# Kernel tuning notes

Hardware: AMD Instinct MI355X
Metric: run time of the kernel (lower is better)

## Reference

```python
import jax, jax.numpy as jnp
import numpy as np

BATCH = 16384
IN_F = 768
OUT_F = 768
GRID_SIZE = 8           # act_fun.get_size()
GRID_LO, GRID_HI = -2.0, 2.0


def rbf_basis(x):
    """Gaussian RBF spline basis: [b, i] -> [b, a, i]."""
    grid = jnp.linspace(GRID_LO, GRID_HI, GRID_SIZE, dtype=x.dtype)  # [a]
    h = (GRID_HI - GRID_LO) / (GRID_SIZE - 1)
    z = (x[:, None, :] - grid[None, :, None]) / h                    # [b, a, i]
    return jnp.exp(-z * z)


def setup_inputs() -> dict:
    key = jax.random.key(0)
    k1, k2, k3 = jax.random.split(key, 3)
    x = jax.random.normal(k1, (BATCH, IN_F), dtype=jnp.float32)
    # xavier_normal_(gain=0.001): std = 0.001 * sqrt(2 / (fan_in + fan_out))
    std_wb = 0.001 * np.sqrt(2.0 / (IN_F + OUT_F))
    w_b = jax.random.normal(k2, (OUT_F, IN_F), dtype=jnp.float32) * std_wb
    w_s = jnp.ones((OUT_F, IN_F), dtype=jnp.float32)
    c = jax.random.normal(k3, (GRID_SIZE, OUT_F, IN_F), dtype=jnp.float32) * 0.001
    return {"x": x, "w_b": w_b, "w_s": w_s, "c": c}


def reference(x, w_b, w_s, c):
    # Original: sum_i[ (sum_a phi(x)_{bai} c_{aoi}) * w_s_{oi} + silu(x)_{bi} * w_b_{oi} ]
    phi = rbf_basis(x)                       # [b, a, i]
    cw = c * w_s[None, :, :]                 # fold scale into coeffs: [a, o, i]
    spline = jnp.einsum('bai,aoi->bo', phi, cw)   # fused contraction over (a, i)
    res = jax.nn.silu(x) @ w_b.T             # [b, o]
    return spline + res
```

## Files before the change

kernel.cpp:

```cpp
#include <hip/hip_runtime.h>
#include <hip/hip_bf16.h>

#define BATCH 16384
#define INF 768
#define OUTF 768
#define NSLAB 9
#define KTOT (NSLAB * INF)
#define BM 128
#define BN 128
#define BK 64
#define KB_TILES 12
#define NTILES (NSLAB * KB_TILES)

#define LOG2E 1.4426950408889634f
#define EXPM2 0.13533528323661270f

#define TILE_SH 8192
#define IB_SH   8192
#define SLAB_SH (KB_TILES * TILE_SH)

typedef __bf16 bf16x8 __attribute__((ext_vector_type(8)));
typedef float f32x4 __attribute__((ext_vector_type(4)));
typedef unsigned short ushort8v __attribute__((ext_vector_type(8)));

__device__ __forceinline__ unsigned short f2bf(float f) {
  unsigned u = __builtin_bit_cast(unsigned, f);
  u += 0x7fffu + ((u >> 16) & 1u);
  return (unsigned short)(u >> 16);
}

__device__ __forceinline__ unsigned cvt2(float a, float b) {
  __hip_bfloat162 h = __float22bfloat162_rn(make_float2(a, b));
  unsigned r;
  __builtin_memcpy(&r, &h, 4);
  return r;
}

__device__ __forceinline__ bf16x8 pack8(const f32x4 a, const f32x4 b) {
  union { uint4 u; bf16x8 v; } r;
  r.u.x = cvt2(a[0], a[1]); r.u.y = cvt2(a[2], a[3]);
  r.u.z = cvt2(b[0], b[1]); r.u.w = cvt2(b[2], b[3]);
  return r.v;
}

__device__ __forceinline__ void gload_lds16(const void* g, void* l) {
  __builtin_amdgcn_global_load_lds(
      (const __attribute__((address_space(1))) unsigned int*)g,
      (__attribute__((address_space(3))) unsigned int*)l, 16, 0, 0);
}

__global__ __launch_bounds__(256) void build_bext2(
    const float* __restrict__ w_b, const float* __restrict__ w_s,
    const float* __restrict__ c, unsigned short* __restrict__ bt) {
  const int gid = blockIdx.x * 256 + threadIdx.x;
  const int lane = gid & 63;
  const int q = (gid >> 6) & 3;
  const int wv = (gid >> 8) & 3;
  const int tile = gid >> 10;
  const int kt = tile % NTILES;
  const int cbq = tile / NTILES;
  const int a = kt / KB_TILES;
  const int ib = kt - a * KB_TILES;
  const int rg = lane >> 3, chh = lane & 7;
  const int o = cbq * 128 + wv * 32 + q * 8 + rg;
  const int i = ib * 64 + (chh ^ rg) * 8;

  float4 v0, v1;
  if (a < 8) {
    const float* cp = c + ((size_t)(a * OUTF + o)) * INF + i;
    const float* wp = w_s + (size_t)o * INF + i;
    const float4 c0 = *(const float4*)cp, c1 = *(const float4*)(cp + 4);
    const float4 s0 = *(const float4*)wp, s1 = *(const float4*)(wp + 4);
    v0 = make_float4(c0.x * s0.x, c0.y * s0.y, c0.z * s0.z, c0.w * s0.w);
    v1 = make_float4(c1.x * s1.x, c1.y * s1.y, c1.z * s1.z, c1.w * s1.w);
  } else {
    const float* bp = w_b + (size_t)o * INF + i;
    v0 = *(const float4*)bp;
    v1 = *(const float4*)(bp + 4);
  }
  ushort8v r;
  r[0] = f2bf(v0.x); r[1] = f2bf(v0.y); r[2] = f2bf(v0.z); r[3] = f2bf(v0.w);
  r[4] = f2bf(v1.x); r[5] = f2bf(v1.y); r[6] = f2bf(v1.z); r[7] = f2bf(v1.w);
  *(ushort8v*)(bt + (size_t)gid * 8) = r;
}

__global__ __launch_bounds__(256, 2) void kan_gemm7(
    const float* __restrict__ x, const unsigned short* __restrict__ bt,
    float* __restrict__ out) {
  __shared__ unsigned short Bs[3][BN * BK];

  const int orig = blockIdx.x;
  const int bid = (orig & 7) * 96 + (orig >> 3);
  const int cb = bid / (BATCH / BM);
  const int rb = bid - cb * (BATCH / BM);
  const int row0 = rb * BM, col0 = cb * BN;

  const int t = threadIdx.x;
  const int lane = t & 63;
  const int w = t >> 6;
  const int lrow = lane & 15, lhi = lane >> 4;

  f32x4 acc[2][8];
#pragma unroll
  for (int mt = 0; mt < 2; ++mt)
#pragma unroll
    for (int n = 0; n < 8; ++n)
      acc[mt][n] = (f32x4){0.f, 0.f, 0.f, 0.f};

  const unsigned short* gt =
      bt + (size_t)cb * NTILES * TILE_SH + w * 2048 + lane * 8;
  const float* xb = x + (size_t)(row0 + w * 32 + lrow) * INF;

  const int c0 = lhi ^ (lrow & 7);
  const int c1 = (4 + lhi) ^ (lrow & 7);
  const unsigned short* pB0 = &Bs[0][lrow * 64 + c0 * 8];
  const unsigned short* pB1 = &Bs[0][lrow * 64 + c1 * 8];

  f32x4 ph[2][2][2], gg[2][2][2];

  auto stage = [&](const unsigned short* src, int slot) {
#pragma unroll
    for (int q = 0; q < 4; ++q)
      gload_lds16(src + q * 512, &Bs[slot][w * 2048 + q * 512]);
  };

  auto mma_kk = [&](int kk, int slot, bf16x8 af0, bf16x8 af1) {
    const unsigned short* pB = kk ? pB1 : pB0;
#pragma unroll
    for (int n = 0; n < 8; ++n) {
      const bf16x8 b = *(const bf16x8*)(pB + slot * TILE_SH + n * 1024);
      acc[0][n] = __builtin_amdgcn_mfma_f32_16x16x32_bf16(af0, b, acc[0][n], 0, 0, 0);
      acc[1][n] = __builtin_amdgcn_mfma_f32_16x16x32_bf16(af1, b, acc[1][n], 0, 0, 0);
    }
  };

  const unsigned short* gib = gt;
  stage(gib + 8 * SLAB_SH, 0);
  stage(gib, 1);
  asm volatile("s_waitcnt vmcnt(4)" ::: "memory");
  __builtin_amdgcn_s_barrier();
  __builtin_amdgcn_sched_barrier(0);

#pragma clang loop unroll(disable)
  for (int ib = 0; ib < KB_TILES; ++ib) {
    const float* xib = xb + ib * BK;
    const bool last = (ib == KB_TILES - 1);
#pragma unroll
    for (int j = 0; j < 9; ++j) {
      const int slot = j % 3;

      if (j == 0) {
        f32x4 xr[4][2];
#pragma unroll
        for (int g = 0; g < 4; ++g) {
          const float* p = xib + (g >> 1) * 16 * INF + (g & 1) * 32 + lhi * 8;
          xr[g][0] = *(const f32x4*)p;
          xr[g][1] = *(const f32x4*)(p + 4);
        }
        stage(gib + 1 * SLAB_SH, 2);
#pragma unroll
        for (int kk = 0; kk < 2; ++kk) {
          bf16x8 af[2];
#pragma unroll
          for (int mt = 0; mt < 2; ++mt) {
            const f32x4 x0 = xr[mt * 2 + kk][0], x1 = xr[mt * 2 + kk][1];
            f32x4 s0, s1;
#pragma unroll
            for (int e = 0; e < 4; ++e) {
              s0[e] = x0[e] * __builtin_amdgcn_rcpf(
                          1.f + __builtin_amdgcn_exp2f(x0[e] * (-LOG2E)));
              s1[e] = x1[e] * __builtin_amdgcn_rcpf(
                          1.f + __builtin_amdgcn_exp2f(x1[e] * (-LOG2E)));
            }
            af[mt] = pack8(s0, s1);
            const f32x4 z0 = x0 * 1.75f + 3.5f;
            const f32x4 z1 = x1 * 1.75f + 3.5f;
#pragma unroll
            for (int e = 0; e < 4; ++e) {
              ph[mt][kk][0][e] = __builtin_amdgcn_exp2f(-(z0[e] * z0[e]) * LOG2E);
              ph[mt][kk][1][e] = __builtin_amdgcn_exp2f(-(z1[e] * z1[e]) * LOG2E);
              gg[mt][kk][0][e] = __builtin_amdgcn_exp2f(z0[e] * (2.f * LOG2E) - LOG2E);
              gg[mt][kk][1][e] = __builtin_amdgcn_exp2f(z1[e] * (2.f * LOG2E) - LOG2E);
            }
          }
          mma_kk(kk, 0, af[0], af[1]);
        }
      } else {
        if (j <= 6) {
          stage(gib + (j + 1) * SLAB_SH, (j + 2) % 3);
        } else if (!last) {
          if (j == 7) stage(gib + 8 * SLAB_SH + IB_SH, 0);
          else        stage(gib + IB_SH, 1);
        }
#pragma unroll
        for (int kk = 0; kk < 2; ++kk) {
          bf16x8 af[2];
#pragma unroll
          for (int mt = 0; mt < 2; ++mt) {
            af[mt] = pack8(ph[mt][kk][0], ph[mt][kk][1]);
            ph[mt][kk][0] *= gg[mt][kk][0];
            ph[mt][kk][1] *= gg[mt][kk][1];
            gg[mt][kk][0] = gg[mt][kk][0] * EXPM2;
            gg[mt][kk][1] = gg[mt][kk][1] * EXPM2;
          }
          mma_kk(kk, slot, af[0], af[1]);
        }
      }

      if (!last || j < 7) {
        asm volatile("s_waitcnt vmcnt(4)" ::: "memory");
      } else if (j == 7) {
        asm volatile("s_waitcnt vmcnt(0)" ::: "memory");
      }
      if (!(last && j == 8)) {
        __builtin_amdgcn_s_barrier();
        __builtin_amdgcn_sched_barrier(0);
      }
    }
    gib += IB_SH;
  }

#pragma unroll
  for (int mt = 0; mt < 2; ++mt) {
#pragma unroll
    for (int n = 0; n < 8; ++n) {
      const int row = row0 + w * 32 + mt * 16 + lhi * 4;
      const int col = col0 + n * 16 + lrow;
#pragma unroll
      for (int r = 0; r < 4; ++r)
        out[(size_t)(row + r) * OUTF + col] = acc[mt][n][r];
    }
  }
}

__device__ __forceinline__ float phi_f(float x, float g) {
  float z = (x - g) * 1.75f;
  return __expf(-z * z);
}
__device__ __forceinline__ float silu_f(float x) {
  return x / (1.f + __expf(-x));
}

__global__ __launch_bounds__(256, 2) void kan_gemm_fb(
    const float* __restrict__ x, const float* __restrict__ w_b,
    const float* __restrict__ w_s, const float* __restrict__ c,
    float* __restrict__ out) {
  __shared__ unsigned short As[128][72];
  __shared__ unsigned short Bs[128][72];

  const int bid = blockIdx.x;
  const int cbf = bid % (OUTF / 128);
  const int rbf = bid / (OUTF / 128);
  const int row0 = rbf * 128, col0 = cbf * 128;

  const int t = threadIdx.x;
  const int lane = t & 63;
  const int w = t >> 6;
  const int wr = w >> 1, wc = w & 1;
  const int lrow = lane & 15, lhi = lane >> 4;

  f32x4 acc[4][4];
#pragma unroll
  for (int m = 0; m < 4; ++m)
#pragma unroll
    for (int n = 0; n < 4; ++n)
      acc[m][n] = (f32x4){0.f, 0.f, 0.f, 0.f};

  const int rsub = t >> 4;
  const int k4 = t & 15;

  for (int kt = 0; kt < KTOT / 64; ++kt) {
    const int a = kt / (INF / 64);
    const int i0 = (kt % (INF / 64)) * 64;
    const float ga = -2.f + (float)a * (4.f / 7.f);

#pragma unroll
    for (int p = 0; p < 8; ++p) {
      const int r = p * 16 + rsub;
      const float4 xv = *(const float4*)(x + (size_t)(row0 + r) * INF + i0 + k4 * 4);
      ushort4 av;
      if (a < 8) {
        av.x = f2bf(phi_f(xv.x, ga)); av.y = f2bf(phi_f(xv.y, ga));
        av.z = f2bf(phi_f(xv.z, ga)); av.w = f2bf(phi_f(xv.w, ga));
      } else {
        av.x = f2bf(silu_f(xv.x)); av.y = f2bf(silu_f(xv.y));
        av.z = f2bf(silu_f(xv.z)); av.w = f2bf(silu_f(xv.w));
      }
      *(ushort4*)&As[r][k4 * 4] = av;

      ushort4 bv;
      if (a < 8) {
        const float4 cv = *(const float4*)(c + ((size_t)a * OUTF + col0 + r) * INF + i0 + k4 * 4);
        const float4 wv = *(const float4*)(w_s + (size_t)(col0 + r) * INF + i0 + k4 * 4);
        bv.x = f2bf(cv.x * wv.x); bv.y = f2bf(cv.y * wv.y);
        bv.z = f2bf(cv.z * wv.z); bv.w = f2bf(cv.w * wv.w);
      } else {
        const float4 bbv = *(const float4*)(w_b + (size_t)(col0 + r) * INF + i0 + k4 * 4);
        bv.x = f2bf(bbv.x); bv.y = f2bf(bbv.y);
        bv.z = f2bf(bbv.z); bv.w = f2bf(bbv.w);
      }
      *(ushort4*)&Bs[r][k4 * 4] = bv;
    }
    __syncthreads();

#pragma unroll
    for (int kk = 0; kk < 2; ++kk) {
      bf16x8 af[4], bfr[4];
#pragma unroll
      for (int m = 0; m < 4; ++m)
        af[m] = *(const bf16x8*)&As[wr * 64 + m * 16 + lrow][kk * 32 + lhi * 8];
#pragma unroll
      for (int n = 0; n < 4; ++n)
        bfr[n] = *(const bf16x8*)&Bs[wc * 64 + n * 16 + lrow][kk * 32 + lhi * 8];
#pragma unroll
      for (int m = 0; m < 4; ++m)
#pragma unroll
        for (int n = 0; n < 4; ++n)
          acc[m][n] = __builtin_amdgcn_mfma_f32_16x16x32_bf16(af[m], bfr[n], acc[m][n], 0, 0, 0);
    }
    __syncthreads();
  }

#pragma unroll
  for (int m = 0; m < 4; ++m) {
#pragma unroll
    for (int n = 0; n < 4; ++n) {
      const int row = row0 + wr * 64 + m * 16 + lhi * 4;
      const int col = col0 + wc * 64 + n * 16 + lrow;
#pragma unroll
      for (int r = 0; r < 4; ++r)
        out[(size_t)(row + r) * OUTF + col] = acc[m][n][r];
    }
  }
}

extern "C" void kernel_launch(void* const* d_in, const int* in_sizes, int n_in,
                              void* d_out, int out_size, void* d_ws, size_t ws_size,
                              hipStream_t stream) {
  const float* x   = (const float*)d_in[0];
  const float* w_b = (const float*)d_in[1];
  const float* w_s = (const float*)d_in[2];
  const float* c   = (const float*)d_in[3];
  float* out = (float*)d_out;

  const size_t need = (size_t)OUTF * KTOT * sizeof(unsigned short);
  if (ws_size >= need) {
    unsigned short* bt = (unsigned short*)d_ws;
    build_bext2<<<(OUTF * KTOT / 8) / 256, 256, 0, stream>>>(w_b, w_s, c, bt);
    kan_gemm7<<<(BATCH / BM) * (OUTF / BN), 256, 0, stream>>>(x, bt, out);
  } else {
    kan_gemm_fb<<<(BATCH / 128) * (OUTF / 128), 256, 0, stream>>>(x, w_b, w_s, c, out);
  }
}
```

Baseline: 226.9 us.

## Switch GEMM warp tiling to 2x2 grid with 64x64 per-warp tiles

Reorganizes the four warps from 32-row by 128-column strips into a 2x2 arrangement of 64x64 tiles. Each warp now reads half as many B fragments from shared memory per k-step. In exchange, every x row's RBF basis and SiLU values are computed by two warps instead of one, doubling that elementwise exp work. It also doubles the per-thread basis recurrence registers, which raises register pressure under the two-blocks-per-CU bound.

```diff
diff --git a/kernel.cpp b/kernel.cpp
--- a/kernel.cpp
+++ b/kernel.cpp
@@ -84,7 +84,7 @@
   *(ushort8v*)(bt + (size_t)gid * 8) = r;
 }
 
-__global__ __launch_bounds__(256, 2) void kan_gemm7(
+__global__ __launch_bounds__(256, 2) void kan_gemm8(
     const float* __restrict__ x, const unsigned short* __restrict__ bt,
     float* __restrict__ out) {
   __shared__ unsigned short Bs[3][BN * BK];
@@ -98,25 +98,26 @@
   const int t = threadIdx.x;
   const int lane = t & 63;
   const int w = t >> 6;
+  const int wr = w >> 1, wc = w & 1;
   const int lrow = lane & 15, lhi = lane >> 4;
 
-  f32x4 acc[2][8];
-#pragma unroll
-  for (int mt = 0; mt < 2; ++mt)
-#pragma unroll
-    for (int n = 0; n < 8; ++n)
+  f32x4 acc[4][4];
+#pragma unroll
+  for (int mt = 0; mt < 4; ++mt)
+#pragma unroll
+    for (int n = 0; n < 4; ++n)
       acc[mt][n] = (f32x4){0.f, 0.f, 0.f, 0.f};
 
   const unsigned short* gt =
       bt + (size_t)cb * NTILES * TILE_SH + w * 2048 + lane * 8;
-  const float* xb = x + (size_t)(row0 + w * 32 + lrow) * INF;
+  const float* xb = x + (size_t)(row0 + wr * 64 + lrow) * INF;
 
   const int c0 = lhi ^ (lrow & 7);
   const int c1 = (4 + lhi) ^ (lrow & 7);
-  const unsigned short* pB0 = &Bs[0][lrow * 64 + c0 * 8];
-  const unsigned short* pB1 = &Bs[0][lrow * 64 + c1 * 8];
-
-  f32x4 ph[2][2][2], gg[2][2][2];
+  const unsigned short* pB0 = &Bs[0][(wc * 64 + lrow) * 64 + c0 * 8];
+  const unsigned short* pB1 = &Bs[0][(wc * 64 + lrow) * 64 + c1 * 8];
+
+  f32x4 ph[4][2][2], gg[4][2][2];
 
   auto stage = [&](const unsigned short* src, int slot) {
 #pragma unroll
@@ -124,13 +125,14 @@
       gload_lds16(src + q * 512, &Bs[slot][w * 2048 + q * 512]);
   };
 
-  auto mma_kk = [&](int kk, int slot, bf16x8 af0, bf16x8 af1) {
+  auto mma_kk = [&](int kk, int slot, const bf16x8* af) {
     const unsigned short* pB = kk ? pB1 : pB0;
 #pragma unroll
-    for (int n = 0; n < 8; ++n) {
+    for (int n = 0; n < 4; ++n) {
       const bf16x8 b = *(const bf16x8*)(pB + slot * TILE_SH + n * 1024);
-      acc[0][n] = __builtin_amdgcn_mfma_f32_16x16x32_bf16(af0, b, acc[0][n], 0, 0, 0);
-      acc[1][n] = __builtin_amdgcn_mfma_f32_16x16x32_bf16(af1, b, acc[1][n], 0, 0, 0);
+#pragma unroll
+      for (int mt = 0; mt < 4; ++mt)
+        acc[mt][n] = __builtin_amdgcn_mfma_f32_16x16x32_bf16(af[mt], b, acc[mt][n], 0, 0, 0);
     }
   };
 
@@ -150,20 +152,22 @@
       const int slot = j % 3;
 
       if (j == 0) {
-        f32x4 xr[4][2];
-#pragma unroll
-        for (int g = 0; g < 4; ++g) {
-          const float* p = xib + (g >> 1) * 16 * INF + (g & 1) * 32 + lhi * 8;
-          xr[g][0] = *(const f32x4*)p;
-          xr[g][1] = *(const f32x4*)(p + 4);
-        }
+        f32x4 xr[4][2][2];
+#pragma unroll
+        for (int mt = 0; mt < 4; ++mt)
+#pragma unroll
+          for (int kk = 0; kk < 2; ++kk) {
+            const float* p = xib + mt * 16 * INF + kk * 32 + lhi * 8;
+            xr[mt][kk][0] = *(const f32x4*)p;
+            xr[mt][kk][1] = *(const f32x4*)(p + 4);
+          }
         stage(gib + 1 * SLAB_SH, 2);
 #pragma unroll
         for (int kk = 0; kk < 2; ++kk) {
-          bf16x8 af[2];
-#pragma unroll
-          for (int mt = 0; mt < 2; ++mt) {
-            const f32x4 x0 = xr[mt * 2 + kk][0], x1 = xr[mt * 2 + kk][1];
+          bf16x8 af[4];
+#pragma unroll
+          for (int mt = 0; mt < 4; ++mt) {
+            const f32x4 x0 = xr[mt][kk][0], x1 = xr[mt][kk][1];
             f32x4 s0, s1;
 #pragma unroll
             for (int e = 0; e < 4; ++e) {
@@ -183,7 +187,7 @@
               gg[mt][kk][1][e] = __builtin_amdgcn_exp2f(z1[e] * (2.f * LOG2E) - LOG2E);
             }
           }
-          mma_kk(kk, 0, af[0], af[1]);
+          mma_kk(kk, 0, af);
         }
       } else {
         if (j <= 6) {
@@ -194,16 +198,16 @@
         }
 #pragma unroll
         for (int kk = 0; kk < 2; ++kk) {
-          bf16x8 af[2];
-#pragma unroll
-          for (int mt = 0; mt < 2; ++mt) {
+          bf16x8 af[4];
+#pragma unroll
+          for (int mt = 0; mt < 4; ++mt) {
             af[mt] = pack8(ph[mt][kk][0], ph[mt][kk][1]);
             ph[mt][kk][0] *= gg[mt][kk][0];
             ph[mt][kk][1] *= gg[mt][kk][1];
             gg[mt][kk][0] = gg[mt][kk][0] * EXPM2;
             gg[mt][kk][1] = gg[mt][kk][1] * EXPM2;
           }
-          mma_kk(kk, slot, af[0], af[1]);
+          mma_kk(kk, slot, af);
         }
       }
 
@@ -221,11 +225,11 @@
   }
 
 #pragma unroll
-  for (int mt = 0; mt < 2; ++mt) {
-#pragma unroll
-    for (int n = 0; n < 8; ++n) {
-      const int row = row0 + w * 32 + mt * 16 + lhi * 4;
-      const int col = col0 + n * 16 + lrow;
+  for (int mt = 0; mt < 4; ++mt) {
+#pragma unroll
+    for (int n = 0; n < 4; ++n) {
+      const int row = row0 + wr * 64 + mt * 16 + lhi * 4;
+      const int col = col0 + wc * 64 + n * 16 + lrow;
 #pragma unroll
       for (int r = 0; r < 4; ++r)
         out[(size_t)(row + r) * OUTF + col] = acc[mt][n][r];
@@ -347,7 +351,7 @@
   if (ws_size >= need) {
     unsigned short* bt = (unsigned short*)d_ws;
     build_bext2<<<(OUTF * KTOT / 8) / 256, 256, 0, stream>>>(w_b, w_s, c, bt);
-    kan_gemm7<<<(BATCH / BM) * (OUTF / BN), 256, 0, stream>>>(x, bt, out);
+    kan_gemm8<<<(BATCH / BM) * (OUTF / BN), 256, 0, stream>>>(x, bt, out);
   } else {
     kan_gemm_fb<<<(BATCH / 128) * (OUTF / 128), 256, 0, stream>>>(x, w_b, w_s, c, out);
   }
```

Result: slower. 459.7 us (+102.6%).

## Software-pipeline A-fragment generation and x loads one step ahead of MFMAs

Applied to the files above, without the earlier changes.

Moves the x loads for the next K-block into the last slab step and computes the SiLU/RBF A-fragments for the next step after the current MFMAs, so the basis math for step j+1 overlaps the matrix ops of step j instead of sitting serially in front of them. The x load latency is also hidden behind the j==8 MFMAs rather than exposed at j==0. It also replaces the bf16 pair conversion with a single v_cvt_pk_bf16_f32 inline asm instruction. The cost is extra live registers for the prefetched x values and the precomputed fragments, which could pressure the 2-waves-per-SIMD occupancy target.

```diff
diff --git a/kernel.cpp b/kernel.cpp
--- a/kernel.cpp
+++ b/kernel.cpp
@@ -30,9 +30,8 @@
 }
 
 __device__ __forceinline__ unsigned cvt2(float a, float b) {
-  __hip_bfloat162 h = __float22bfloat162_rn(make_float2(a, b));
   unsigned r;
-  __builtin_memcpy(&r, &h, 4);
+  asm("v_cvt_pk_bf16_f32 %0, %1, %2" : "=v"(r) : "v"(a), "v"(b));
   return r;
 }
 
@@ -84,7 +83,7 @@
   *(ushort8v*)(bt + (size_t)gid * 8) = r;
 }
 
-__global__ __launch_bounds__(256, 2) void kan_gemm7(
+__global__ __launch_bounds__(256, 2) void kan_gemm9(
     const float* __restrict__ x, const unsigned short* __restrict__ bt,
     float* __restrict__ out) {
   __shared__ unsigned short Bs[3][BN * BK];
@@ -117,6 +116,7 @@
   const unsigned short* pB1 = &Bs[0][lrow * 64 + c1 * 8];
 
   f32x4 ph[2][2][2], gg[2][2][2];
+  bf16x8 afc[2][2];
 
   auto stage = [&](const unsigned short* src, int slot) {
 #pragma unroll
@@ -124,88 +124,96 @@
       gload_lds16(src + q * 512, &Bs[slot][w * 2048 + q * 512]);
   };
 
-  auto mma_kk = [&](int kk, int slot, bf16x8 af0, bf16x8 af1) {
+  auto mma_kk = [&](int kk, int slot) {
     const unsigned short* pB = kk ? pB1 : pB0;
 #pragma unroll
     for (int n = 0; n < 8; ++n) {
       const bf16x8 b = *(const bf16x8*)(pB + slot * TILE_SH + n * 1024);
-      acc[0][n] = __builtin_amdgcn_mfma_f32_16x16x32_bf16(af0, b, acc[0][n], 0, 0, 0);
-      acc[1][n] = __builtin_amdgcn_mfma_f32_16x16x32_bf16(af1, b, acc[1][n], 0, 0, 0);
-    }
-  };
-
+      acc[0][n] = __builtin_amdgcn_mfma_f32_16x16x32_bf16(afc[kk][0], b, acc[0][n], 0, 0, 0);
+      acc[1][n] = __builtin_amdgcn_mfma_f32_16x16x32_bf16(afc[kk][1], b, acc[1][n], 0, 0, 0);
+    }
+  };
+
+  f32x4 xr[2][2][2];
+  auto load_x = [&](int ib) {
+#pragma unroll
+    for (int mt = 0; mt < 2; ++mt)
+#pragma unroll
+      for (int kk = 0; kk < 2; ++kk) {
+        const float* p = xb + ib * BK + mt * 16 * INF + kk * 32 + lhi * 8;
+        xr[mt][kk][0] = *(const f32x4*)p;
+        xr[mt][kk][1] = *(const f32x4*)(p + 4);
+      }
+  };
+  auto silu_init = [&]() {
+#pragma unroll
+    for (int kk = 0; kk < 2; ++kk)
+#pragma unroll
+      for (int mt = 0; mt < 2; ++mt) {
+        const f32x4 x0 = xr[mt][kk][0], x1 = xr[mt][kk][1];
+        f32x4 s0, s1;
+#pragma unroll
+        for (int e = 0; e < 4; ++e) {
+          s0[e] = x0[e] * __builtin_amdgcn_rcpf(
+                      1.f + __builtin_amdgcn_exp2f(x0[e] * (-LOG2E)));
+          s1[e] = x1[e] * __builtin_amdgcn_rcpf(
+                      1.f + __builtin_amdgcn_exp2f(x1[e] * (-LOG2E)));
+        }
+        afc[kk][mt] = pack8(s0, s1);
+        const f32x4 z0 = x0 * 1.75f + 3.5f;
+        const f32x4 z1 = x1 * 1.75f + 3.5f;
+#pragma unroll
+        for (int e = 0; e < 4; ++e) {
+          ph[mt][kk][0][e] = __builtin_amdgcn_exp2f(-(z0[e] * z0[e]) * LOG2E);
+          ph[mt][kk][1][e] = __builtin_amdgcn_exp2f(-(z1[e] * z1[e]) * LOG2E);
+          gg[mt][kk][0][e] = __builtin_amdgcn_exp2f(z0[e] * (2.f * LOG2E) - LOG2E);
+          gg[mt][kk][1][e] = __builtin_amdgcn_exp2f(z1[e] * (2.f * LOG2E) - LOG2E);
+        }
+      }
+  };
+  auto pack_advance = [&]() {
+#pragma unroll
+    for (int kk = 0; kk < 2; ++kk)
+#pragma unroll
+      for (int mt = 0; mt < 2; ++mt) {
+        afc[kk][mt] = pack8(ph[mt][kk][0], ph[mt][kk][1]);
+        ph[mt][kk][0] *= gg[mt][kk][0];
+        ph[mt][kk][1] *= gg[mt][kk][1];
+        gg[mt][kk][0] = gg[mt][kk][0] * EXPM2;
+        gg[mt][kk][1] = gg[mt][kk][1] * EXPM2;
+      }
+  };
+
+  load_x(0);
   const unsigned short* gib = gt;
   stage(gib + 8 * SLAB_SH, 0);
   stage(gib, 1);
+  silu_init();
   asm volatile("s_waitcnt vmcnt(4)" ::: "memory");
   __builtin_amdgcn_s_barrier();
   __builtin_amdgcn_sched_barrier(0);
 
 #pragma clang loop unroll(disable)
   for (int ib = 0; ib < KB_TILES; ++ib) {
-    const float* xib = xb + ib * BK;
     const bool last = (ib == KB_TILES - 1);
 #pragma unroll
     for (int j = 0; j < 9; ++j) {
       const int slot = j % 3;
 
-      if (j == 0) {
-        f32x4 xr[4][2];
-#pragma unroll
-        for (int g = 0; g < 4; ++g) {
-          const float* p = xib + (g >> 1) * 16 * INF + (g & 1) * 32 + lhi * 8;
-          xr[g][0] = *(const f32x4*)p;
-          xr[g][1] = *(const f32x4*)(p + 4);
-        }
-        stage(gib + 1 * SLAB_SH, 2);
-#pragma unroll
-        for (int kk = 0; kk < 2; ++kk) {
-          bf16x8 af[2];
-#pragma unroll
-          for (int mt = 0; mt < 2; ++mt) {
-            const f32x4 x0 = xr[mt * 2 + kk][0], x1 = xr[mt * 2 + kk][1];
-            f32x4 s0, s1;
-#pragma unroll
-            for (int e = 0; e < 4; ++e) {
-              s0[e] = x0[e] * __builtin_amdgcn_rcpf(
-                          1.f + __builtin_amdgcn_exp2f(x0[e] * (-LOG2E)));
-              s1[e] = x1[e] * __builtin_amdgcn_rcpf(
-                          1.f + __builtin_amdgcn_exp2f(x1[e] * (-LOG2E)));
-            }
-            af[mt] = pack8(s0, s1);
-            const f32x4 z0 = x0 * 1.75f + 3.5f;
-            const f32x4 z1 = x1 * 1.75f + 3.5f;
-#pragma unroll
-            for (int e = 0; e < 4; ++e) {
-              ph[mt][kk][0][e] = __builtin_amdgcn_exp2f(-(z0[e] * z0[e]) * LOG2E);
-              ph[mt][kk][1][e] = __builtin_amdgcn_exp2f(-(z1[e] * z1[e]) * LOG2E);
-              gg[mt][kk][0][e] = __builtin_amdgcn_exp2f(z0[e] * (2.f * LOG2E) - LOG2E);
-              gg[mt][kk][1][e] = __builtin_amdgcn_exp2f(z1[e] * (2.f * LOG2E) - LOG2E);
-            }
-          }
-          mma_kk(kk, 0, af[0], af[1]);
-        }
-      } else {
-        if (j <= 6) {
-          stage(gib + (j + 1) * SLAB_SH, (j + 2) % 3);
-        } else if (!last) {
-          if (j == 7) stage(gib + 8 * SLAB_SH + IB_SH, 0);
-          else        stage(gib + IB_SH, 1);
-        }
-#pragma unroll
-        for (int kk = 0; kk < 2; ++kk) {
-          bf16x8 af[2];
-#pragma unroll
-          for (int mt = 0; mt < 2; ++mt) {
-            af[mt] = pack8(ph[mt][kk][0], ph[mt][kk][1]);
-            ph[mt][kk][0] *= gg[mt][kk][0];
-            ph[mt][kk][1] *= gg[mt][kk][1];
-            gg[mt][kk][0] = gg[mt][kk][0] * EXPM2;
-            gg[mt][kk][1] = gg[mt][kk][1] * EXPM2;
-          }
-          mma_kk(kk, slot, af[0], af[1]);
-        }
-      }
+      if (j == 8 && !last) load_x(ib + 1);
+
+      if (j <= 6) {
+        stage(gib + (j + 1) * SLAB_SH, (j + 2) % 3);
+      } else if (!last) {
+        if (j == 7) stage(gib + 8 * SLAB_SH + IB_SH, 0);
+        else        stage(gib + IB_SH, 1);
+      }
+
+      mma_kk(0, slot);
+      mma_kk(1, slot);
+
+      if (j < 8)       pack_advance();
+      else if (!last)  silu_init();
 
       if (!last || j < 7) {
         asm volatile("s_waitcnt vmcnt(4)" ::: "memory");
@@ -347,7 +355,7 @@
   if (ws_size >= need) {
     unsigned short* bt = (unsigned short*)d_ws;
     build_bext2<<<(OUTF * KTOT / 8) / 256, 256, 0, stream>>>(w_b, w_s, c, bt);
-    kan_gemm7<<<(BATCH / BM) * (OUTF / BN), 256, 0, stream>>>(x, bt, out);
+    kan_gemm9<<<(BATCH / BM) * (OUTF / BN), 256, 0, stream>>>(x, bt, out);
   } else {
     kan_gemm_fb<<<(BATCH / 128) * (OUTF / 128), 256, 0, stream>>>(x, w_b, w_s, c, out);
   }
```

New measurement: 202.0 us (median of 2 runs). -11.0%, faster.
